# Kernel tuning notes

Measured on AMD Instinct MI355X. Metric: run time of the kernel, lower is better.

## Reference

```python
import jax, jax.numpy as jnp
import numpy as np

B, H, L, D = 2, 16, 2048, 64

def setup_inputs() -> dict:
    key = jax.random.key(0)
    kq, kk, kv, km = jax.random.split(key, 4)
    q = jax.random.normal(kq, (B, H, L, D), dtype=jnp.float32)
    k = jax.random.normal(kk, (B, H, L, D), dtype=jnp.float32)
    v = jax.random.normal(kv, (B, H, L, D), dtype=jnp.float32)
    mask = jax.random.randint(km, (B, 1, L, L), 0, 2, dtype=jnp.int32)
    return {"q": q, "k": k, "v": v, "mask": mask}

def reference(q, k, v, mask):
    d_tensor = q.shape[-1]
    # score: [B,H,L,L] = q @ k^T / sqrt(d)
    score = jnp.einsum("bhqd,bhkd->bhqk", q, k) / jnp.sqrt(jnp.float32(d_tensor))
    score = jnp.where(mask == 0, jnp.float32(-jnp.inf), score)
    score = jax.nn.softmax(score, axis=-1)
    # torch.nan_to_num(nan=0.0): rows fully masked produce NaN -> 0
    score = jnp.where(jnp.isnan(score), jnp.float32(0.0), score)
    # dropout=0.0 (eval / p=0) -> identity
    out = jnp.einsum("bhqk,bhkd->bhqd", score, v)
    return (out, score)
```

## Files before the change

### kernel.cpp

```cpp
#include <hip/hip_runtime.h>
#include <math.h>

#define B_ 2
#define H_ 16
#define L_ 2048
#define D_ 64
#define OUT_ELEMS ((size_t)B_ * H_ * L_ * D_)
#define WPR (L_ / 16)
#define C1 0.180336880f

typedef _Float16 half8 __attribute__((ext_vector_type(8)));
typedef _Float16 half4_t __attribute__((ext_vector_type(4)));
typedef float f32x4 __attribute__((ext_vector_type(4)));
typedef int i32x4 __attribute__((ext_vector_type(4)));
typedef unsigned int u32;
typedef unsigned short u16;
typedef u16 u16x4 __attribute__((ext_vector_type(4)));
typedef u32 u32x4 __attribute__((ext_vector_type(4)));
typedef u32 u32x2 __attribute__((ext_vector_type(2)));

#define SWZ(row, colh) ((colh) ^ (((row) & 7) << 3))

__global__ __launch_bounds__(256) void pack_kernel(
    const int* __restrict__ M, u16* __restrict__ pmask)
{
  const int idx = blockIdx.x * 256 + threadIdx.x;
  const int* src = M + (size_t)idx * 16;
  u32 w = 0;
#pragma unroll
  for (int j = 0; j < 4; ++j) {
    i32x4 m = ((const i32x4*)src)[j];
#pragma unroll
    for (int r = 0; r < 4; ++r)
      w |= (m[r] != 0 ? 1u : 0u) << (j * 4 + r);
  }
  pmask[idx] = (u16)w;
}

__global__ __launch_bounds__(256, 8) void lsum_kernel(
    const float* __restrict__ Q, const float* __restrict__ K,
    const u16* __restrict__ pmask, float* __restrict__ lpart)
{
  const int qt = blockIdx.x, h = blockIdx.y;
  const int b = blockIdx.z >> 2, kq = blockIdx.z & 3;
  const int bh = b * H_ + h;
  const int q0 = qt * 64, k0 = kq * 512;
  const int tid = threadIdx.x;
  const int wv = tid >> 6, lane = tid & 63;
  const int lr = lane & 15, lg = lane >> 4;
  const int qrow = q0 + wv * 16 + lr;

  __shared__ _Float16 Kbuf[64 * 64];

  const float* kbase = K + ((size_t)bh * L_ + k0) * D_;
  const u16* pmrow = pmask + (size_t)(b * L_ + qrow) * WPR + (k0 >> 4);

  half8 qf[2];
  {
    const float* qr = Q + (size_t)(bh * L_ + qrow) * D_;
#pragma unroll
    for (int f = 0; f < 2; ++f) {
      f32x4 x = *(const f32x4*)(qr + f * 32 + lg * 8);
      f32x4 y = *(const f32x4*)(qr + f * 32 + lg * 8 + 4);
      qf[f] = half8{(_Float16)(x[0]*C1), (_Float16)(x[1]*C1), (_Float16)(x[2]*C1), (_Float16)(x[3]*C1),
                    (_Float16)(y[0]*C1), (_Float16)(y[1]*C1), (_Float16)(y[2]*C1), (_Float16)(y[3]*C1)};
    }
  }

  const int ksr = tid >> 2, ksd = (tid & 3) * 16;
  float l_l = 0.f;

  for (int c = 0; c < 8; ++c) {
    const int kc = c * 64;
    f32x4 kr[4];
    {
      const float* s = kbase + (size_t)(kc + ksr) * D_ + ksd;
      kr[0] = ((const f32x4*)s)[0]; kr[1] = ((const f32x4*)s)[1];
      kr[2] = ((const f32x4*)s)[2]; kr[3] = ((const f32x4*)s)[3];
    }
    __syncthreads();
    {
      half8 lo = half8{(_Float16)kr[0][0], (_Float16)kr[0][1], (_Float16)kr[0][2], (_Float16)kr[0][3],
                       (_Float16)kr[1][0], (_Float16)kr[1][1], (_Float16)kr[1][2], (_Float16)kr[1][3]};
      half8 hi = half8{(_Float16)kr[2][0], (_Float16)kr[2][1], (_Float16)kr[2][2], (_Float16)kr[2][3],
                       (_Float16)kr[3][0], (_Float16)kr[3][1], (_Float16)kr[3][2], (_Float16)kr[3][3]};
      *(half8*)&Kbuf[(ksr << 6) + SWZ(ksr, ksd)] = lo;
      *(half8*)&Kbuf[(ksr << 6) + SWZ(ksr, ksd + 8)] = hi;
    }
    __syncthreads();

    u16x4 pm = *(const u16x4*)(pmrow + c * 4);
    f32x4 acc[4] = {f32x4{0,0,0,0}, f32x4{0,0,0,0}, f32x4{0,0,0,0}, f32x4{0,0,0,0}};
    __builtin_amdgcn_s_setprio(1);
#pragma unroll
    for (int kb = 0; kb < 4; ++kb) {
      int row = kb * 16 + lr;
      half8 a0 = *(const half8*)&Kbuf[(row << 6) + SWZ(row, lg * 8)];
      half8 a1 = *(const half8*)&Kbuf[(row << 6) + SWZ(row, 32 + lg * 8)];
      acc[kb] = __builtin_amdgcn_mfma_f32_16x16x32_f16(a0, qf[0], acc[kb], 0, 0, 0);
      acc[kb] = __builtin_amdgcn_mfma_f32_16x16x32_f16(a1, qf[1], acc[kb], 0, 0, 0);
    }
    __builtin_amdgcn_s_setprio(0);

    float cs = 0.f;
#pragma unroll
    for (int kb = 0; kb < 4; ++kb)
#pragma unroll
      for (int r = 0; r < 4; ++r)
        cs += exp2f(((pm[kb] >> (lg * 4 + r)) & 1) ? acc[kb][r] : -INFINITY);
    l_l += cs;
  }

  l_l += __shfl_xor(l_l, 16);
  l_l += __shfl_xor(l_l, 32);
  if (lg == 0)
    lpart[((size_t)kq * 32 + bh) * L_ + qrow] = l_l;
}

template <int KCH>
__device__ __forceinline__ void attn_body(
    const float* Q, const float* K, const float* V,
    const u16* pmask, const float* lpart,
    float* obase, float* score, int b, int h, int qt, int k0)
{
  const int bh = b * H_ + h;
  const int q0 = qt * 64;
  const int tid = threadIdx.x;
  const int wv = tid >> 6, lane = tid & 63;
  const int lr = lane & 15, lg = lane >> 4;
  const int qrow = q0 + wv * 16 + lr;

  __shared__ _Float16 Klds[2][64 * 64];
  __shared__ _Float16 Vlds[2][64 * 64];

  const float* kbase = K + ((size_t)bh * L_ + k0) * D_;
  const float* vbase = V + ((size_t)bh * L_ + k0) * D_;
  const u16* pmrow = pmask + (size_t)(b * L_ + qrow) * WPR + (k0 >> 4);
  float* srow = score + ((size_t)bh * L_ + qrow) * L_ + k0;
  float* ob = obase + (size_t)(bh * L_ + q0) * D_;

  float lsum = 0.f;
#pragma unroll
  for (int kq = 0; kq < 4; ++kq)
    lsum += lpart[((size_t)kq * 32 + bh) * L_ + qrow];
  const float inv_l = (lsum > 0.f) ? 1.f / lsum : 0.f;

  half8 qf[2];
  {
    const float* qr = Q + (size_t)(bh * L_ + qrow) * D_;
#pragma unroll
    for (int f = 0; f < 2; ++f) {
      f32x4 x = *(const f32x4*)(qr + f * 32 + lg * 8);
      f32x4 y = *(const f32x4*)(qr + f * 32 + lg * 8 + 4);
      qf[f] = half8{(_Float16)(x[0]*C1), (_Float16)(x[1]*C1), (_Float16)(x[2]*C1), (_Float16)(x[3]*C1),
                    (_Float16)(y[0]*C1), (_Float16)(y[1]*C1), (_Float16)(y[2]*C1), (_Float16)(y[3]*C1)};
    }
  }

  const int ksr = tid >> 2, ksd = (tid & 3) * 16;
  const int vk0 = (tid & 15) * 4, vd0 = (tid >> 4) * 4;

  auto loadK4 = [&](int kc, f32x4* r) {
    const float* s = kbase + (size_t)(kc + ksr) * D_ + ksd;
    r[0] = ((const f32x4*)s)[0]; r[1] = ((const f32x4*)s)[1];
    r[2] = ((const f32x4*)s)[2]; r[3] = ((const f32x4*)s)[3];
  };
  auto writeK = [&](int buf, const f32x4* r) {
    half8 lo = half8{(_Float16)r[0][0], (_Float16)r[0][1], (_Float16)r[0][2], (_Float16)r[0][3],
                     (_Float16)r[1][0], (_Float16)r[1][1], (_Float16)r[1][2], (_Float16)r[1][3]};
    half8 hi = half8{(_Float16)r[2][0], (_Float16)r[2][1], (_Float16)r[2][2], (_Float16)r[2][3],
                     (_Float16)r[3][0], (_Float16)r[3][1], (_Float16)r[3][2], (_Float16)r[3][3]};
    *(half8*)&Klds[buf][(ksr << 6) + SWZ(ksr, ksd)] = lo;
    *(half8*)&Klds[buf][(ksr << 6) + SWZ(ksr, ksd + 8)] = hi;
  };
  auto loadV4 = [&](int kc, f32x4* r) {
#pragma unroll
    for (int i = 0; i < 4; ++i)
      r[i] = *(const f32x4*)(vbase + (size_t)(kc + vk0 + i) * D_ + vd0);
  };
  auto writeV = [&](int buf, const f32x4* r) {
#pragma unroll
    for (int j = 0; j < 4; ++j) {
      int row = vd0 + j;
      *(half4_t*)&Vlds[buf][(row << 6) + SWZ(row, vk0)] =
          half4_t{(_Float16)r[0][j], (_Float16)r[1][j],
                  (_Float16)r[2][j], (_Float16)r[3][j]};
    }
  };

  {
    f32x4 kr[4], vr[4];
    loadK4(0, kr); loadV4(0, vr);
    writeK(0, kr); writeV(0, vr);
  }
  __syncthreads();

  f32x4 o_acc[4] = {f32x4{0,0,0,0}, f32x4{0,0,0,0}, f32x4{0,0,0,0}, f32x4{0,0,0,0}};

  const int s0lane = lr + 32 * (lg & 1);
  const int s1lane = s0lane + 16;
  const bool hisel = (lg & 2) != 0;

  for (int c = 0; c < KCH; ++c) {
    const int kc = c * 64, cur = c & 1;
    f32x4 krP[4], vrP[4];
    if (c < KCH - 1) {
      loadK4(kc + 64, krP);
      loadV4(kc + 64, vrP);
    }
    u16x4 pm = *(const u16x4*)(pmrow + c * 4);

    f32x4 acc[4] = {f32x4{0,0,0,0}, f32x4{0,0,0,0}, f32x4{0,0,0,0}, f32x4{0,0,0,0}};
    __builtin_amdgcn_s_setprio(1);
#pragma unroll
    for (int kb = 0; kb < 4; ++kb) {
      int row = kb * 16 + lr;
      half8 a0 = *(const half8*)&Klds[cur][(row << 6) + SWZ(row, lg * 8)];
      half8 a1 = *(const half8*)&Klds[cur][(row << 6) + SWZ(row, 32 + lg * 8)];
      acc[kb] = __builtin_amdgcn_mfma_f32_16x16x32_f16(a0, qf[0], acc[kb], 0, 0, 0);
      acc[kb] = __builtin_amdgcn_mfma_f32_16x16x32_f16(a1, qf[1], acc[kb], 0, 0, 0);
    }
    __builtin_amdgcn_s_setprio(0);

    u32 phu[8];
#pragma unroll
    for (int kb = 0; kb < 4; ++kb) {
      f32x4 p4;
#pragma unroll
      for (int r = 0; r < 4; ++r)
        p4[r] = exp2f(((pm[kb] >> (lg * 4 + r)) & 1) ? acc[kb][r] : -INFINITY) * inv_l;
      __builtin_nontemporal_store(p4, (f32x4*)(srow + kc + kb * 16 + lg * 4));
      half4_t hp = half4_t{(_Float16)p4[0], (_Float16)p4[1],
                           (_Float16)p4[2], (_Float16)p4[3]};
      u32x2 uu = __builtin_bit_cast(u32x2, hp);
      phu[2 * kb] = uu[0];
      phu[2 * kb + 1] = uu[1];
    }

    __builtin_amdgcn_s_setprio(1);
#pragma unroll
    for (int ks = 0; ks < 2; ++ks) {
      int a0 = __shfl((int)phu[4 * ks + 0], s0lane);
      int a1 = __shfl((int)phu[4 * ks + 1], s0lane);
      int a2 = __shfl((int)phu[4 * ks + 2], s0lane);
      int a3 = __shfl((int)phu[4 * ks + 3], s0lane);
      int b0 = __shfl((int)phu[4 * ks + 0], s1lane);
      int b1 = __shfl((int)phu[4 * ks + 1], s1lane);
      int b2 = __shfl((int)phu[4 * ks + 2], s1lane);
      int b3 = __shfl((int)phu[4 * ks + 3], s1lane);
      u32x4 pau = u32x4{(u32)(hisel ? a2 : a0), (u32)(hisel ? a3 : a1),
                        (u32)(hisel ? b2 : b0), (u32)(hisel ? b3 : b1)};
      half8 pa = __builtin_bit_cast(half8, pau);
#pragma unroll
      for (int db = 0; db < 4; ++db) {
        int row = db * 16 + lr;
        half8 vf = *(const half8*)&Vlds[cur][(row << 6) + SWZ(row, ks * 32 + lg * 8)];
        o_acc[db] = __builtin_amdgcn_mfma_f32_16x16x32_f16(pa, vf, o_acc[db], 0, 0, 0);
      }
    }
    __builtin_amdgcn_s_setprio(0);

    if (c < KCH - 1) {
      writeK(cur ^ 1, krP);
      writeV(cur ^ 1, vrP);
    }
    __syncthreads();
  }

#pragma unroll
  for (int db = 0; db < 4; ++db)
#pragma unroll
    for (int r = 0; r < 4; ++r)
      ob[(size_t)(wv * 16 + lg * 4 + r) * D_ + db * 16 + lr] = o_acc[db][r];
}

__global__ __launch_bounds__(256, 4) void attn_split_kernel(
    const float* __restrict__ Q, const float* __restrict__ K,
    const float* __restrict__ V, const u16* __restrict__ pmask,
    const float* __restrict__ lpart,
    float* __restrict__ op0, float* __restrict__ op1, float* __restrict__ score)
{
  const int bid = blockIdx.x;
  const int lid = (bid & 7) * (2048 / 8) + (bid >> 3);
  const int qt = lid & 31, kh = (lid >> 5) & 1, h = (lid >> 6) & 15, b = lid >> 10;
  attn_body<16>(Q, K, V, pmask, lpart, kh ? op1 : op0, score,
                b, h, qt, kh * 1024);
}

__global__ __launch_bounds__(256, 4) void attn_full_kernel(
    const float* __restrict__ Q, const float* __restrict__ K,
    const float* __restrict__ V, const u16* __restrict__ pmask,
    const float* __restrict__ lpart,
    float* __restrict__ out, float* __restrict__ score)
{
  const int bid = blockIdx.x;
  const int lid = (bid & 7) * (1024 / 8) + (bid >> 3);
  const int qt = lid & 31, h = (lid >> 5) & 15, b = lid >> 9;
  attn_body<32>(Q, K, V, pmask, lpart, out, score, b, h, qt, 0);
}

__global__ __launch_bounds__(256) void combine_kernel(
    const float* __restrict__ op1, float* __restrict__ out)
{
  const int idx = blockIdx.x * 256 + threadIdx.x;
  f32x4 a = ((const f32x4*)out)[idx];
  f32x4 bq = ((const f32x4*)op1)[idx];
  a[0] += bq[0]; a[1] += bq[1]; a[2] += bq[2]; a[3] += bq[3];
  __builtin_nontemporal_store(a, (f32x4*)out + idx);
}

extern "C" void kernel_launch(void* const* d_in, const int* in_sizes, int n_in,
                              void* d_out, int out_size, void* d_ws, size_t ws_size,
                              hipStream_t stream) {
  const float* q = (const float*)d_in[0];
  const float* k = (const float*)d_in[1];
  const float* v = (const float*)d_in[2];
  const int* mask = (const int*)d_in[3];
  float* out = (float*)d_out;
  float* score = out + OUT_ELEMS;

  u16* pmask = (u16*)d_ws;
  float* lpart = (float*)((char*)d_ws + (1 << 20));
  float* op1 = (float*)((char*)d_ws + (2 << 20));
  const size_t need = (size_t)(2 << 20) + OUT_ELEMS * sizeof(float);

  pack_kernel<<<dim3(B_ * L_ * WPR / 256), 256, 0, stream>>>(mask, pmask);
  lsum_kernel<<<dim3(32, 16, 8), 256, 0, stream>>>(q, k, pmask, lpart);
  if (ws_size >= need) {
    attn_split_kernel<<<dim3(2048), 256, 0, stream>>>(q, k, v, pmask, lpart,
                                                      out, op1, score);
    combine_kernel<<<dim3(OUT_ELEMS / 4 / 256), 256, 0, stream>>>(op1, out);
  } else {
    attn_full_kernel<<<dim3(1024), 256, 0, stream>>>(q, k, v, pmask, lpart,
                                                     out, score);
  }
}
```

Measured before the change: 242.2 us.

## Use 512-thread blocks covering 128 query rows, splitting K/V staging across halves

Doubles the block to 8 waves handling 128 query rows, so each staged K/V tile in LDS is reused by twice as many rows. The load work is split: the first 256 threads load and convert K while the second 256 handle V, halving per-thread prefetch registers. Grid sizes and block index decoding are halved to match, and launch bounds change to (512, 8). This raises per-block synchronization cost and changes occupancy.

After: 525.5 us. 117% more time.

```diff
diff --git a/kernel.cpp b/kernel.cpp
--- a/kernel.cpp
+++ b/kernel.cpp
@@ -124,11 +124,13 @@
     float* obase, float* score, int b, int h, int qt, int k0)
 {
   const int bh = b * H_ + h;
-  const int q0 = qt * 64;
+  const int q0 = qt * 128;
   const int tid = threadIdx.x;
   const int wv = tid >> 6, lane = tid & 63;
   const int lr = lane & 15, lg = lane >> 4;
   const int qrow = q0 + wv * 16 + lr;
+  const bool kgrp = tid < 256;
+  const int t2 = tid & 255;
 
   __shared__ _Float16 Klds[2][64 * 64];
   __shared__ _Float16 Vlds[2][64 * 64];
@@ -157,41 +159,43 @@
     }
   }
 
-  const int ksr = tid >> 2, ksd = (tid & 3) * 16;
-  const int vk0 = (tid & 15) * 4, vd0 = (tid >> 4) * 4;
-
-  auto loadK4 = [&](int kc, f32x4* r) {
-    const float* s = kbase + (size_t)(kc + ksr) * D_ + ksd;
-    r[0] = ((const f32x4*)s)[0]; r[1] = ((const f32x4*)s)[1];
-    r[2] = ((const f32x4*)s)[2]; r[3] = ((const f32x4*)s)[3];
+  const int ksr = t2 >> 2, ksd = (t2 & 3) * 16;
+  const int vk0 = (t2 & 15) * 4, vd0 = (t2 >> 4) * 4;
+
+  auto loadKV = [&](int kc, f32x4* r) {
+    if (kgrp) {
+      const float* s = kbase + (size_t)(kc + ksr) * D_ + ksd;
+      r[0] = ((const f32x4*)s)[0]; r[1] = ((const f32x4*)s)[1];
+      r[2] = ((const f32x4*)s)[2]; r[3] = ((const f32x4*)s)[3];
+    } else {
+#pragma unroll
+      for (int i = 0; i < 4; ++i)
+        r[i] = *(const f32x4*)(vbase + (size_t)(kc + vk0 + i) * D_ + vd0);
+    }
   };
-  auto writeK = [&](int buf, const f32x4* r) {
-    half8 lo = half8{(_Float16)r[0][0], (_Float16)r[0][1], (_Float16)r[0][2], (_Float16)r[0][3],
-                     (_Float16)r[1][0], (_Float16)r[1][1], (_Float16)r[1][2], (_Float16)r[1][3]};
-    half8 hi = half8{(_Float16)r[2][0], (_Float16)r[2][1], (_Float16)r[2][2], (_Float16)r[2][3],
-                     (_Float16)r[3][0], (_Float16)r[3][1], (_Float16)r[3][2], (_Float16)r[3][3]};
-    *(half8*)&Klds[buf][(ksr << 6) + SWZ(ksr, ksd)] = lo;
-    *(half8*)&Klds[buf][(ksr << 6) + SWZ(ksr, ksd + 8)] = hi;
+  auto writeKV = [&](int buf, const f32x4* r) {
+    if (kgrp) {
+      half8 lo = half8{(_Float16)r[0][0], (_Float16)r[0][1], (_Float16)r[0][2], (_Float16)r[0][3],
+                       (_Float16)r[1][0], (_Float16)r[1][1], (_Float16)r[1][2], (_Float16)r[1][3]};
+      half8 hi = half8{(_Float16)r[2][0], (_Float16)r[2][1], (_Float16)r[2][2], (_Float16)r[2][3],
+                       (_Float16)r[3][0], (_Float16)r[3][1], (_Float16)r[3][2], (_Float16)r[3][3]};
+      *(half8*)&Klds[buf][(ksr << 6) + SWZ(ksr, ksd)] = lo;
+      *(half8*)&Klds[buf][(ksr << 6) + SWZ(ksr, ksd + 8)] = hi;
+    } else {
+#pragma unroll
+      for (int j = 0; j < 4; ++j) {
+        int row = vd0 + j;
+        *(half4_t*)&Vlds[buf][(row << 6) + SWZ(row, vk0)] =
+            half4_t{(_Float16)r[0][j], (_Float16)r[1][j],
+                    (_Float16)r[2][j], (_Float16)r[3][j]};
+      }
+    }
   };
-  auto loadV4 = [&](int kc, f32x4* r) {
-#pragma unroll
-    for (int i = 0; i < 4; ++i)
-      r[i] = *(const f32x4*)(vbase + (size_t)(kc + vk0 + i) * D_ + vd0);
-  };
-  auto writeV = [&](int buf, const f32x4* r) {
-#pragma unroll
-    for (int j = 0; j < 4; ++j) {
-      int row = vd0 + j;
-      *(half4_t*)&Vlds[buf][(row << 6) + SWZ(row, vk0)] =
-          half4_t{(_Float16)r[0][j], (_Float16)r[1][j],
-                  (_Float16)r[2][j], (_Float16)r[3][j]};
-    }
-  };
 
   {
-    f32x4 kr[4], vr[4];
-    loadK4(0, kr); loadV4(0, vr);
-    writeK(0, kr); writeV(0, vr);
+    f32x4 r0[4];
+    loadKV(0, r0);
+    writeKV(0, r0);
   }
   __syncthreads();
 
@@ -203,11 +207,8 @@
 
   for (int c = 0; c < KCH; ++c) {
     const int kc = c * 64, cur = c & 1;
-    f32x4 krP[4], vrP[4];
-    if (c < KCH - 1) {
-      loadK4(kc + 64, krP);
-      loadV4(kc + 64, vrP);
-    }
+    f32x4 rP[4];
+    if (c < KCH - 1) loadKV(kc + 64, rP);
     u16x4 pm = *(const u16x4*)(pmrow + c * 4);
 
     f32x4 acc[4] = {f32x4{0,0,0,0}, f32x4{0,0,0,0}, f32x4{0,0,0,0}, f32x4{0,0,0,0}};
@@ -260,10 +261,7 @@
     }
     __builtin_amdgcn_s_setprio(0);
 
-    if (c < KCH - 1) {
-      writeK(cur ^ 1, krP);
-      writeV(cur ^ 1, vrP);
-    }
+    if (c < KCH - 1) writeKV(cur ^ 1, rP);
     __syncthreads();
   }
 
@@ -274,28 +272,28 @@
       ob[(size_t)(wv * 16 + lg * 4 + r) * D_ + db * 16 + lr] = o_acc[db][r];
 }
 
-__global__ __launch_bounds__(256, 4) void attn_split_kernel(
+__global__ __launch_bounds__(512, 8) void attn_split_kernel(
     const float* __restrict__ Q, const float* __restrict__ K,
     const float* __restrict__ V, const u16* __restrict__ pmask,
     const float* __restrict__ lpart,
     float* __restrict__ op0, float* __restrict__ op1, float* __restrict__ score)
 {
   const int bid = blockIdx.x;
-  const int lid = (bid & 7) * (2048 / 8) + (bid >> 3);
-  const int qt = lid & 31, kh = (lid >> 5) & 1, h = (lid >> 6) & 15, b = lid >> 10;
+  const int lid = (bid & 7) * (1024 / 8) + (bid >> 3);
+  const int qt = lid & 15, kh = (lid >> 4) & 1, h = (lid >> 5) & 15, b = lid >> 9;
   attn_body<16>(Q, K, V, pmask, lpart, kh ? op1 : op0, score,
                 b, h, qt, kh * 1024);
 }
 
-__global__ __launch_bounds__(256, 4) void attn_full_kernel(
+__global__ __launch_bounds__(512, 8) void attn_full_kernel(
     const float* __restrict__ Q, const float* __restrict__ K,
     const float* __restrict__ V, const u16* __restrict__ pmask,
     const float* __restrict__ lpart,
     float* __restrict__ out, float* __restrict__ score)
 {
   const int bid = blockIdx.x;
-  const int lid = (bid & 7) * (1024 / 8) + (bid >> 3);
-  const int qt = lid & 31, h = (lid >> 5) & 15, b = lid >> 9;
+  const int lid = (bid & 7) * (512 / 8) + (bid >> 3);
+  const int qt = lid & 15, h = (lid >> 4) & 15, b = lid >> 8;
   attn_body<32>(Q, K, V, pmask, lpart, out, score, b, h, qt, 0);
 }
 
@@ -327,11 +325,11 @@
   pack_kernel<<<dim3(B_ * L_ * WPR / 256), 256, 0, stream>>>(mask, pmask);
   lsum_kernel<<<dim3(32, 16, 8), 256, 0, stream>>>(q, k, pmask, lpart);
   if (ws_size >= need) {
-    attn_split_kernel<<<dim3(2048), 256, 0, stream>>>(q, k, v, pmask, lpart,
+    attn_split_kernel<<<dim3(1024), 512, 0, stream>>>(q, k, v, pmask, lpart,
                                                       out, op1, score);
     combine_kernel<<<dim3(OUT_ELEMS / 4 / 256), 256, 0, stream>>>(op1, out);
   } else {
-    attn_full_kernel<<<dim3(1024), 256, 0, stream>>>(q, k, v, pmask, lpart,
-                                                     out, score);
-  }
-}
+    attn_full_kernel<<<dim3(512), 512, 0, stream>>>(q, k, v, pmask, lpart,
+                                                    out, score);
+  }
+}
```

## Replace double-buffered K/V LDS staging with single buffer and raise occupancy

Applied to the files above, without the earlier changes.

Drops the register-prefetch double buffer for K/V tiles. Each chunk now loads K/V from global, syncs, writes one shared buffer, syncs again, then computes. This halves LDS use and cuts live prefetch registers, so launch bounds rise from 4 to 6 blocks per SIMD/CU. The trade is losing the overlap of global loads with compute and adding a second barrier per chunk, in exchange for more resident waves to hide latency.

After: 261.4 us. 1.08x slower.

```diff
diff --git a/kernel.cpp b/kernel.cpp
--- a/kernel.cpp
+++ b/kernel.cpp
@@ -130,8 +130,8 @@
   const int lr = lane & 15, lg = lane >> 4;
   const int qrow = q0 + wv * 16 + lr;
 
-  __shared__ _Float16 Klds[2][64 * 64];
-  __shared__ _Float16 Vlds[2][64 * 64];
+  __shared__ _Float16 Klds[64 * 64];
+  __shared__ _Float16 Vlds[64 * 64];
 
   const float* kbase = K + ((size_t)bh * L_ + k0) * D_;
   const float* vbase = V + ((size_t)bh * L_ + k0) * D_;
@@ -160,41 +160,6 @@
   const int ksr = tid >> 2, ksd = (tid & 3) * 16;
   const int vk0 = (tid & 15) * 4, vd0 = (tid >> 4) * 4;
 
-  auto loadK4 = [&](int kc, f32x4* r) {
-    const float* s = kbase + (size_t)(kc + ksr) * D_ + ksd;
-    r[0] = ((const f32x4*)s)[0]; r[1] = ((const f32x4*)s)[1];
-    r[2] = ((const f32x4*)s)[2]; r[3] = ((const f32x4*)s)[3];
-  };
-  auto writeK = [&](int buf, const f32x4* r) {
-    half8 lo = half8{(_Float16)r[0][0], (_Float16)r[0][1], (_Float16)r[0][2], (_Float16)r[0][3],
-                     (_Float16)r[1][0], (_Float16)r[1][1], (_Float16)r[1][2], (_Float16)r[1][3]};
-    half8 hi = half8{(_Float16)r[2][0], (_Float16)r[2][1], (_Float16)r[2][2], (_Float16)r[2][3],
-                     (_Float16)r[3][0], (_Float16)r[3][1], (_Float16)r[3][2], (_Float16)r[3][3]};
-    *(half8*)&Klds[buf][(ksr << 6) + SWZ(ksr, ksd)] = lo;
-    *(half8*)&Klds[buf][(ksr << 6) + SWZ(ksr, ksd + 8)] = hi;
-  };
-  auto loadV4 = [&](int kc, f32x4* r) {
-#pragma unroll
-    for (int i = 0; i < 4; ++i)
-      r[i] = *(const f32x4*)(vbase + (size_t)(kc + vk0 + i) * D_ + vd0);
-  };
-  auto writeV = [&](int buf, const f32x4* r) {
-#pragma unroll
-    for (int j = 0; j < 4; ++j) {
-      int row = vd0 + j;
-      *(half4_t*)&Vlds[buf][(row << 6) + SWZ(row, vk0)] =
-          half4_t{(_Float16)r[0][j], (_Float16)r[1][j],
-                  (_Float16)r[2][j], (_Float16)r[3][j]};
-    }
-  };
-
-  {
-    f32x4 kr[4], vr[4];
-    loadK4(0, kr); loadV4(0, vr);
-    writeK(0, kr); writeV(0, vr);
-  }
-  __syncthreads();
-
   f32x4 o_acc[4] = {f32x4{0,0,0,0}, f32x4{0,0,0,0}, f32x4{0,0,0,0}, f32x4{0,0,0,0}};
 
   const int s0lane = lr + 32 * (lg & 1);
@@ -202,12 +167,35 @@
   const bool hisel = (lg & 2) != 0;
 
   for (int c = 0; c < KCH; ++c) {
-    const int kc = c * 64, cur = c & 1;
-    f32x4 krP[4], vrP[4];
-    if (c < KCH - 1) {
-      loadK4(kc + 64, krP);
-      loadV4(kc + 64, vrP);
-    }
+    const int kc = c * 64;
+    f32x4 kr[4], vr[4];
+    {
+      const float* s = kbase + (size_t)(kc + ksr) * D_ + ksd;
+      kr[0] = ((const f32x4*)s)[0]; kr[1] = ((const f32x4*)s)[1];
+      kr[2] = ((const f32x4*)s)[2]; kr[3] = ((const f32x4*)s)[3];
+    }
+#pragma unroll
+    for (int i = 0; i < 4; ++i)
+      vr[i] = *(const f32x4*)(vbase + (size_t)(kc + vk0 + i) * D_ + vd0);
+
+    __syncthreads();
+    {
+      half8 lo = half8{(_Float16)kr[0][0], (_Float16)kr[0][1], (_Float16)kr[0][2], (_Float16)kr[0][3],
+                       (_Float16)kr[1][0], (_Float16)kr[1][1], (_Float16)kr[1][2], (_Float16)kr[1][3]};
+      half8 hi = half8{(_Float16)kr[2][0], (_Float16)kr[2][1], (_Float16)kr[2][2], (_Float16)kr[2][3],
+                       (_Float16)kr[3][0], (_Float16)kr[3][1], (_Float16)kr[3][2], (_Float16)kr[3][3]};
+      *(half8*)&Klds[(ksr << 6) + SWZ(ksr, ksd)] = lo;
+      *(half8*)&Klds[(ksr << 6) + SWZ(ksr, ksd + 8)] = hi;
+    }
+#pragma unroll
+    for (int j = 0; j < 4; ++j) {
+      int row = vd0 + j;
+      *(half4_t*)&Vlds[(row << 6) + SWZ(row, vk0)] =
+          half4_t{(_Float16)vr[0][j], (_Float16)vr[1][j],
+                  (_Float16)vr[2][j], (_Float16)vr[3][j]};
+    }
+    __syncthreads();
+
     u16x4 pm = *(const u16x4*)(pmrow + c * 4);
 
     f32x4 acc[4] = {f32x4{0,0,0,0}, f32x4{0,0,0,0}, f32x4{0,0,0,0}, f32x4{0,0,0,0}};
@@ -215,8 +203,8 @@
 #pragma unroll
     for (int kb = 0; kb < 4; ++kb) {
       int row = kb * 16 + lr;
-      half8 a0 = *(const half8*)&Klds[cur][(row << 6) + SWZ(row, lg * 8)];
-      half8 a1 = *(const half8*)&Klds[cur][(row << 6) + SWZ(row, 32 + lg * 8)];
+      half8 a0 = *(const half8*)&Klds[(row << 6) + SWZ(row, lg * 8)];
+      half8 a1 = *(const half8*)&Klds[(row << 6) + SWZ(row, 32 + lg * 8)];
       acc[kb] = __builtin_amdgcn_mfma_f32_16x16x32_f16(a0, qf[0], acc[kb], 0, 0, 0);
       acc[kb] = __builtin_amdgcn_mfma_f32_16x16x32_f16(a1, qf[1], acc[kb], 0, 0, 0);
     }
@@ -254,17 +242,11 @@
 #pragma unroll
       for (int db = 0; db < 4; ++db) {
         int row = db * 16 + lr;
-        half8 vf = *(const half8*)&Vlds[cur][(row << 6) + SWZ(row, ks * 32 + lg * 8)];
+        half8 vf = *(const half8*)&Vlds[(row << 6) + SWZ(row, ks * 32 + lg * 8)];
         o_acc[db] = __builtin_amdgcn_mfma_f32_16x16x32_f16(pa, vf, o_acc[db], 0, 0, 0);
       }
     }
     __builtin_amdgcn_s_setprio(0);
-
-    if (c < KCH - 1) {
-      writeK(cur ^ 1, krP);
-      writeV(cur ^ 1, vrP);
-    }
-    __syncthreads();
   }
 
 #pragma unroll
@@ -274,7 +256,7 @@
       ob[(size_t)(wv * 16 + lg * 4 + r) * D_ + db * 16 + lr] = o_acc[db][r];
 }
 
-__global__ __launch_bounds__(256, 4) void attn_split_kernel(
+__global__ __launch_bounds__(256, 6) void attn_split_kernel(
     const float* __restrict__ Q, const float* __restrict__ K,
     const float* __restrict__ V, const u16* __restrict__ pmask,
     const float* __restrict__ lpart,
@@ -287,7 +269,7 @@
                 b, h, qt, kh * 1024);
 }
 
-__global__ __launch_bounds__(256, 4) void attn_full_kernel(
+__global__ __launch_bounds__(256, 6) void attn_full_kernel(
     const float* __restrict__ Q, const float* __restrict__ K,
     const float* __restrict__ V, const u16* __restrict__ pmask,
     const float* __restrict__ lpart,
```
